# Optimization experiments

Hardware: AMD Instinct MI355X
Metric: run time of the kernel (lower is better)

## Reference

```python
import jax, jax.numpy as jnp
import numpy as np

TEMPERATURE = 0.02


def setup_inputs() -> dict:
    key = jax.random.key(0)
    k1, k2 = jax.random.split(key)
    B, D_PER, DIM = 4096, 2, 1024
    # scale embeddings so sim/temperature stays in a sane range (like normalized embeddings)
    scale = 1.0 / np.sqrt(DIM)
    query_embeds = jax.random.normal(k1, (B, DIM), dtype=jnp.float32) * scale
    doc_embeds = jax.random.normal(k2, (B * D_PER, DIM), dtype=jnp.float32) * scale
    return {
        "query_embeds": query_embeds,
        "doc_embeds": doc_embeds,
        "num_docs_per_sample": D_PER,
    }


def reference(query_embeds, doc_embeds, num_docs_per_sample):
    # Single-device path of the original: all_doc_embeds == doc_embeds,
    # local_rank == 0, pos_global_idx = i * num_docs_per_sample.
    B = query_embeds.shape[0]
    # [B, total_docs] similarity matrix (one batched GEMM instead of per-sample loop)
    logits = (query_embeds @ doc_embeds.T) / TEMPERATURE
    pos_idx = jnp.arange(B) * num_docs_per_sample  # constant docs-per-sample offsets
    pos_logit = jnp.take_along_axis(logits, pos_idx[:, None], axis=1)[:, 0]
    lse = jax.nn.logsumexp(logits, axis=1)
    loss = jnp.sum(lse - pos_logit) / B
    return loss
```

## Files before the change

kernel.cpp:

```cpp
#include <hip/hip_runtime.h>


#define TEMP_INV 50.0f
#define PRESCALE 16.0f
#define SCALE_BYTE 123

typedef int   i32x4 __attribute__((ext_vector_type(4)));
typedef int   i32x8 __attribute__((ext_vector_type(8)));
typedef float f32x4 __attribute__((ext_vector_type(4)));

__global__ void cvt_kernel(const float* __restrict__ Q, const float* __restrict__ Dm,
                           unsigned int* __restrict__ Q8, unsigned int* __restrict__ D8,
                           float* __restrict__ rowsum, int qSlots, int B, int K) {
    const int gid = blockIdx.x * blockDim.x + threadIdx.x;
    if (gid < B) rowsum[gid] = 0.0f;
    const float* src;
    unsigned int* dst;
    int s;
    if (gid < qSlots) { src = Q;  dst = Q8; s = gid; }
    else              { src = Dm; dst = D8; s = gid - qSlots; }
    {
        const int l0 = s & 63;
        s = (s & ~63) | (((l0 & 3) << 4) | (l0 >> 2));
    }
    const int l   = s & 63;
    const int c   = (s >> 6) & 15;
    const int k0b = (s >> 10) & 7;
    const int R   = s >> 13;
    const int row = R * 128 + (c >> 1) * 16 + (l & 15);
    const int k   = k0b * 128 + (c & 1) * 64 + (l >> 4) * 16;
    const float* p = src + (size_t)row * K + k;
    unsigned int w[4];
#pragma unroll
    for (int d = 0; d < 4; ++d) {
        float4 v = *(const float4*)(p + d * 4);
        int t = __builtin_amdgcn_cvt_pk_fp8_f32(v.x * PRESCALE, v.y * PRESCALE, 0, false);
        t = __builtin_amdgcn_cvt_pk_fp8_f32(v.z * PRESCALE, v.w * PRESCALE, t, true);
        w[d] = (unsigned int)t;
    }
    *(uint4*)(dst + (size_t)s * 4) = make_uint4(w[0], w[1], w[2], w[3]);
}

__global__ __launch_bounds__(256, 2) void gemm_expsum_kernel(
        const unsigned int* __restrict__ Q8, const unsigned int* __restrict__ D8,
        const int* __restrict__ dper,
        float* __restrict__ rowsum, float* __restrict__ pos, int K) {
    __shared__ unsigned int BUF[12288];

    const int tid   = threadIdx.x;
    const int wave  = tid >> 6;
    const int lane  = tid & 63;
    const int wr    = wave >> 1;
    const int wc    = wave & 1;
    const int lquad = lane >> 4;
    const int lm    = lane & 15;
    const int kh    = lquad >> 1;

    const int f   = blockIdx.x;
    const int xcd = f & 7;
    const int sub = f >> 3;
    const int bx  = (xcd & 1) * 8 + (sub & 7);
    const int by  = (xcd >> 1) * 16 + (sub >> 3);

    const int qbase = bx * 256;
    const int dbase = by * 128;
    const int KB    = K >> 7;

    const unsigned int* QgA = Q8 + (size_t)(2 * bx) * KB * 4096;
    const unsigned int* DgB = D8 + (size_t)by * KB * 4096;

    const int slotofs = ((lquad & 1) * 32 + lm) * 4;
    const int aofs = (wr * 8 * 2 + kh) * 256 + slotofs;
    const int bofs = 8192 + (wc * 8 + kh) * 256 + slotofs;

    f32x4 acc[32];
#pragma unroll
    for (int t = 0; t < 32; ++t) acc[t] = (f32x4){0.f, 0.f, 0.f, 0.f};

#define LDFRAG(dst_, off_) do {                                              \
        i32x4 lo_ = *(const i32x4*)(BUF + (off_));                           \
        i32x4 hi_ = *(const i32x4*)(BUF + (off_) + 64);                      \
        dst_ = __builtin_shufflevector(lo_, hi_, 0, 1, 2, 3, 4, 5, 6, 7);    \
    } while (0)

#define MFMA1(AA, BB, IDX)                                                   \
        acc[IDX] = __builtin_amdgcn_mfma_scale_f32_16x16x128_f8f6f4(         \
            AA, BB, acc[IDX], 0, 0, 0, SCALE_BYTE, 0, SCALE_BYTE)

    for (int kb = 0; kb < KB; ++kb) {
#pragma unroll
        for (int q = 0; q < 8; ++q) {
            const int ca = wave * 8 + q;
            const unsigned int* g = QgA + (size_t)(ca >> 4) * KB * 4096
                                    + kb * 4096 + (ca & 15) * 256 + lane * 4;
            __builtin_amdgcn_global_load_lds(
                (const __attribute__((address_space(1))) void*)g,
                (__attribute__((address_space(3))) void*)(BUF + ca * 256 + lane * 4),
                16, 0, 0);
        }
#pragma unroll
        for (int q = 0; q < 4; ++q) {
            const int cb = wave * 4 + q;
            const unsigned int* g = DgB + kb * 4096 + cb * 256 + lane * 4;
            __builtin_amdgcn_global_load_lds(
                (const __attribute__((address_space(1))) void*)g,
                (__attribute__((address_space(3))) void*)(BUF + 8192 + cb * 256 + lane * 4),
                16, 0, 0);
        }
        __syncthreads();

        i32x8 B0, B1, B2, B3;
        LDFRAG(B0, bofs + 0 * 512);
        LDFRAG(B1, bofs + 1 * 512);
        LDFRAG(B2, bofs + 2 * 512);
        LDFRAG(B3, bofs + 3 * 512);
        {
            i32x8 A0, A1, A2, A3;
            LDFRAG(A0, aofs + 0 * 512);
            LDFRAG(A1, aofs + 1 * 512);
            LDFRAG(A2, aofs + 2 * 512);
            LDFRAG(A3, aofs + 3 * 512);
            MFMA1(A0, B0,  0); MFMA1(A0, B1,  1); MFMA1(A0, B2,  2); MFMA1(A0, B3,  3);
            MFMA1(A1, B0,  4); MFMA1(A1, B1,  5); MFMA1(A1, B2,  6); MFMA1(A1, B3,  7);
            MFMA1(A2, B0,  8); MFMA1(A2, B1,  9); MFMA1(A2, B2, 10); MFMA1(A2, B3, 11);
            MFMA1(A3, B0, 12); MFMA1(A3, B1, 13); MFMA1(A3, B2, 14); MFMA1(A3, B3, 15);
        }
        {
            i32x8 A4, A5, A6, A7;
            LDFRAG(A4, aofs + 4 * 512);
            LDFRAG(A5, aofs + 5 * 512);
            LDFRAG(A6, aofs + 6 * 512);
            LDFRAG(A7, aofs + 7 * 512);
            MFMA1(A4, B0, 16); MFMA1(A4, B1, 17); MFMA1(A4, B2, 18); MFMA1(A4, B3, 19);
            MFMA1(A5, B0, 20); MFMA1(A5, B1, 21); MFMA1(A5, B2, 22); MFMA1(A5, B3, 23);
            MFMA1(A6, B0, 24); MFMA1(A6, B1, 25); MFMA1(A6, B2, 26); MFMA1(A6, B3, 27);
            MFMA1(A7, B0, 28); MFMA1(A7, B1, 29); MFMA1(A7, B2, 30); MFMA1(A7, B3, 31);
        }
        __syncthreads();
    }
#undef MFMA1
#undef LDFRAG

    const int dp = dper[0];
#pragma unroll
    for (int i = 0; i < 8; ++i)
#pragma unroll
        for (int r = 0; r < 4; ++r) {
            const int gr   = qbase + wr * 128 + 16 * i + 4 * lquad + r;
            const int pcol = gr * dp - dbase;
            float e = 0.0f;
#pragma unroll
            for (int j = 0; j < 4; ++j) {
                float v = acc[i * 4 + j][r];
                if (wc * 64 + 16 * j + lm == pcol) pos[gr] = v * TEMP_INV;
                e += __expf(v * TEMP_INV);
            }
            e += __shfl_xor(e, 1);
            e += __shfl_xor(e, 2);
            e += __shfl_xor(e, 4);
            e += __shfl_xor(e, 8);
            if (lm == 0) atomicAdd(&rowsum[gr], e);
        }
}

__global__ void final_kernel(const float* __restrict__ rowsum,
                             const float* __restrict__ pos,
                             float* __restrict__ out, int B) {
    __shared__ float red[16];
    int tid = threadIdx.x;
    float s = 0.0f;
    for (int i = tid; i < B; i += blockDim.x)
        s += __logf(rowsum[i]) - pos[i];
    s += __shfl_xor(s, 32);
    s += __shfl_xor(s, 16);
    s += __shfl_xor(s, 8);
    s += __shfl_xor(s, 4);
    s += __shfl_xor(s, 2);
    s += __shfl_xor(s, 1);
    int w = tid >> 6, l = tid & 63;
    if (l == 0) red[w] = s;
    __syncthreads();
    if (tid == 0) {
        float t = 0.0f;
        int nw = blockDim.x >> 6;
        for (int i = 0; i < nw; ++i) t += red[i];
        out[0] = t / (float)B;
    }
}

extern "C" void kernel_launch(void* const* d_in, const int* in_sizes, int n_in,
                              void* d_out, int out_size, void* d_ws, size_t ws_size,
                              hipStream_t stream) {
    const float* Q   = (const float*)d_in[0];
    const float* Dm  = (const float*)d_in[1];
    const int* dper  = (const int*)d_in[2];
    float* out = (float*)d_out;

    const int DIM  = 1024;
    const int B    = in_sizes[0] / DIM;
    const int Ntot = in_sizes[1] / DIM;

    unsigned int* Q8 = (unsigned int*)d_ws;
    unsigned int* D8 = Q8 + (size_t)B * DIM / 4;
    float* rowsum = (float*)(D8 + (size_t)Ntot * DIM / 4);
    float* pos = rowsum + B;

    const int qSlots = B * DIM / 16;
    const int dSlots = Ntot * DIM / 16;
    cvt_kernel<<<(qSlots + dSlots) / 256, 256, 0, stream>>>(
        Q, Dm, Q8, D8, rowsum, qSlots, B, DIM);

    const int nblk = (B / 256) * (Ntot / 128);
    gemm_expsum_kernel<<<nblk, 256, 0, stream>>>(Q8, D8, dper, rowsum, pos, DIM);

    final_kernel<<<1, 1024, 0, stream>>>(rowsum, pos, out, B);
}
```

Before: 132.9 us.

## Split 256x128 GEMM tile across eight waves instead of four

Doubles the block to 512 threads so each wave computes a 64x64 sub-tile (16 accumulators) instead of 128x64 (32 accumulators). The global-to-LDS copy is redistributed with 6 loads per wave, and the A fragment offsets and epilogue row mapping are updated to match. This lowers per-wave register pressure and gives more waves to hide latency, at the cost of more LDS fragment reads per MFMA and more barrier participants.

```diff
diff --git a/kernel.cpp b/kernel.cpp
--- a/kernel.cpp
+++ b/kernel.cpp
@@ -41,7 +41,7 @@
     *(uint4*)(dst + (size_t)s * 4) = make_uint4(w[0], w[1], w[2], w[3]);
 }
 
-__global__ __launch_bounds__(256, 2) void gemm_expsum_kernel(
+__global__ __launch_bounds__(512, 2) void gemm_expsum_kernel(
         const unsigned int* __restrict__ Q8, const unsigned int* __restrict__ D8,
         const int* __restrict__ dper,
         float* __restrict__ rowsum, float* __restrict__ pos, int K) {
@@ -66,16 +66,13 @@
     const int dbase = by * 128;
     const int KB    = K >> 7;
 
-    const unsigned int* QgA = Q8 + (size_t)(2 * bx) * KB * 4096;
-    const unsigned int* DgB = D8 + (size_t)by * KB * 4096;
-
     const int slotofs = ((lquad & 1) * 32 + lm) * 4;
-    const int aofs = (wr * 8 * 2 + kh) * 256 + slotofs;
+    const int aofs = ((wr >> 1) * 16 + (wr & 1) * 8 + kh) * 256 + slotofs;
     const int bofs = 8192 + (wc * 8 + kh) * 256 + slotofs;
 
-    f32x4 acc[32];
+    f32x4 acc[16];
 #pragma unroll
-    for (int t = 0; t < 32; ++t) acc[t] = (f32x4){0.f, 0.f, 0.f, 0.f};
+    for (int t = 0; t < 16; ++t) acc[t] = (f32x4){0.f, 0.f, 0.f, 0.f};
 
 #define LDFRAG(dst_, off_) do {                                              \
         i32x4 lo_ = *(const i32x4*)(BUF + (off_));                           \
@@ -89,53 +86,35 @@
 
     for (int kb = 0; kb < KB; ++kb) {
 #pragma unroll
-        for (int q = 0; q < 8; ++q) {
-            const int ca = wave * 8 + q;
-            const unsigned int* g = QgA + (size_t)(ca >> 4) * KB * 4096
-                                    + kb * 4096 + (ca & 15) * 256 + lane * 4;
+        for (int q = 0; q < 6; ++q) {
+            const int fl = wave * 6 + q;
+            const unsigned int* g;
+            if (fl < 32)
+                g = Q8 + (size_t)(2 * bx + (fl >> 4)) * (KB * 4096)
+                       + kb * 4096 + (fl & 15) * 256 + lane * 4;
+            else
+                g = D8 + (size_t)by * (KB * 4096)
+                       + kb * 4096 + (fl - 32) * 256 + lane * 4;
             __builtin_amdgcn_global_load_lds(
                 (const __attribute__((address_space(1))) void*)g,
-                (__attribute__((address_space(3))) void*)(BUF + ca * 256 + lane * 4),
-                16, 0, 0);
-        }
-#pragma unroll
-        for (int q = 0; q < 4; ++q) {
-            const int cb = wave * 4 + q;
-            const unsigned int* g = DgB + kb * 4096 + cb * 256 + lane * 4;
-            __builtin_amdgcn_global_load_lds(
-                (const __attribute__((address_space(1))) void*)g,
-                (__attribute__((address_space(3))) void*)(BUF + 8192 + cb * 256 + lane * 4),
+                (__attribute__((address_space(3))) void*)(BUF + fl * 256 + lane * 4),
                 16, 0, 0);
         }
         __syncthreads();
 
-        i32x8 B0, B1, B2, B3;
+        i32x8 B0, B1, B2, B3, A0, A1, A2, A3;
         LDFRAG(B0, bofs + 0 * 512);
         LDFRAG(B1, bofs + 1 * 512);
         LDFRAG(B2, bofs + 2 * 512);
         LDFRAG(B3, bofs + 3 * 512);
-        {
-            i32x8 A0, A1, A2, A3;
-            LDFRAG(A0, aofs + 0 * 512);
-            LDFRAG(A1, aofs + 1 * 512);
-            LDFRAG(A2, aofs + 2 * 512);
-            LDFRAG(A3, aofs + 3 * 512);
-            MFMA1(A0, B0,  0); MFMA1(A0, B1,  1); MFMA1(A0, B2,  2); MFMA1(A0, B3,  3);
-            MFMA1(A1, B0,  4); MFMA1(A1, B1,  5); MFMA1(A1, B2,  6); MFMA1(A1, B3,  7);
-            MFMA1(A2, B0,  8); MFMA1(A2, B1,  9); MFMA1(A2, B2, 10); MFMA1(A2, B3, 11);
-            MFMA1(A3, B0, 12); MFMA1(A3, B1, 13); MFMA1(A3, B2, 14); MFMA1(A3, B3, 15);
-        }
-        {
-            i32x8 A4, A5, A6, A7;
-            LDFRAG(A4, aofs + 4 * 512);
-            LDFRAG(A5, aofs + 5 * 512);
-            LDFRAG(A6, aofs + 6 * 512);
-            LDFRAG(A7, aofs + 7 * 512);
-            MFMA1(A4, B0, 16); MFMA1(A4, B1, 17); MFMA1(A4, B2, 18); MFMA1(A4, B3, 19);
-            MFMA1(A5, B0, 20); MFMA1(A5, B1, 21); MFMA1(A5, B2, 22); MFMA1(A5, B3, 23);
-            MFMA1(A6, B0, 24); MFMA1(A6, B1, 25); MFMA1(A6, B2, 26); MFMA1(A6, B3, 27);
-            MFMA1(A7, B0, 28); MFMA1(A7, B1, 29); MFMA1(A7, B2, 30); MFMA1(A7, B3, 31);
-        }
+        LDFRAG(A0, aofs + 0 * 512);
+        LDFRAG(A1, aofs + 1 * 512);
+        LDFRAG(A2, aofs + 2 * 512);
+        LDFRAG(A3, aofs + 3 * 512);
+        MFMA1(A0, B0,  0); MFMA1(A0, B1,  1); MFMA1(A0, B2,  2); MFMA1(A0, B3,  3);
+        MFMA1(A1, B0,  4); MFMA1(A1, B1,  5); MFMA1(A1, B2,  6); MFMA1(A1, B3,  7);
+        MFMA1(A2, B0,  8); MFMA1(A2, B1,  9); MFMA1(A2, B2, 10); MFMA1(A2, B3, 11);
+        MFMA1(A3, B0, 12); MFMA1(A3, B1, 13); MFMA1(A3, B2, 14); MFMA1(A3, B3, 15);
         __syncthreads();
     }
 #undef MFMA1
@@ -143,10 +122,10 @@
 
     const int dp = dper[0];
 #pragma unroll
-    for (int i = 0; i < 8; ++i)
+    for (int i = 0; i < 4; ++i)
 #pragma unroll
         for (int r = 0; r < 4; ++r) {
-            const int gr   = qbase + wr * 128 + 16 * i + 4 * lquad + r;
+            const int gr   = qbase + wr * 64 + 16 * i + 4 * lquad + r;
             const int pcol = gr * dp - dbase;
             float e = 0.0f;
 #pragma unroll
@@ -211,7 +190,7 @@
         Q, Dm, Q8, D8, rowsum, qSlots, B, DIM);
 
     const int nblk = (B / 256) * (Ntot / 128);
-    gemm_expsum_kernel<<<nblk, 256, 0, stream>>>(Q8, D8, dper, rowsum, pos, DIM);
+    gemm_expsum_kernel<<<nblk, 512, 0, stream>>>(Q8, D8, dper, rowsum, pos, DIM);
 
     final_kernel<<<1, 1024, 0, stream>>>(rowsum, pos, out, B);
 }
```

Result: slower. 143.4 us (+7.9%).
